# Optimization experiments

Measured on AMD Instinct MI355X. Metric: run time of the kernel, lower is better.

Reference implementation:

```python
import jax, jax.numpy as jnp
import numpy as np

D = 256

def setup_inputs() -> dict:
    key = jax.random.key(0)
    k1, k2, k3, k4, k5, k6 = jax.random.split(key, 6)
    M, N = 2048, 512
    s = 1.0 / np.sqrt(D)
    return {
        "q_vec": jax.random.normal(k1, (M, D), dtype=jnp.float32),
        "kv": jax.random.normal(k2, (M, N, D), dtype=jnp.float32),
        "wq": jax.random.uniform(k3, (D, D), jnp.float32, -s, s),
        "wk": jax.random.uniform(k4, (D, D), jnp.float32, -s, s),
        "wv": jax.random.uniform(k5, (D, D), jnp.float32, -s, s),
        "wo": (jax.random.uniform(k6, (D, D), jnp.float32, -s, s)),
    }

def reference(q_vec, kv, wq, wk, wv, wo):
    # q_vec: [M, d], kv: [M, N, d]; weights stored torch-style [out, in] -> apply x @ W.T
    d = q_vec.shape[-1]
    q = q_vec @ wq.T                          # [M, d]
    k = jnp.einsum('mnd,ed->mne', kv, wk)     # [M, N, d]
    v = jnp.einsum('mnd,ed->mne', kv, wv)     # [M, N, d]
    logits = jnp.einsum('md,mnd->mn', q, k) / jnp.sqrt(jnp.float32(d))  # [M, N]
    attn = jax.nn.softmax(logits, axis=-1)    # [M, N] (dropout p=0.0 is identity)
    ctx = jnp.einsum('mn,mnd->md', attn, v)   # [M, d]
    out = ctx @ wo.T                          # [M, d]
    return out, attn
```

## Files before the change

kernel.cpp:

```cpp
#include <hip/hip_runtime.h>
#include <math.h>

#define DD 256
#define MM 2048
#define NN 512

__global__ void prep_weights(const float* __restrict__ wq, const float* __restrict__ wk,
                             const float* __restrict__ wv, const float* __restrict__ wo,
                             float* __restrict__ B1, float* __restrict__ B2T) {
    __shared__ float sA[DD];
    const int j = threadIdx.x;
    const int b = blockIdx.x;
    if (b < DD) {
        const int d = b;
        sA[j] = wq[j * DD + d];
        __syncthreads();
        float acc = 0.f;
        for (int a = 0; a < DD; ++a) acc = fmaf(sA[a], wk[a * DD + j], acc);
        B1[d * DD + j] = acc * 0.0625f;
    } else {
        const int d = b - DD;
        sA[j] = wv[j * DD + d];
        __syncthreads();
        float acc = 0.f;
        for (int e = 0; e < DD; ++e) acc = fmaf(wo[j * DD + e], sA[e], acc);
        B2T[d * DD + j] = acc;
    }
}

__global__ __launch_bounds__(256, 4)
void attn_fused(const float* __restrict__ q_vec, const float* __restrict__ kv,
                const float* __restrict__ B1, const float* __restrict__ B2T,
                float* __restrict__ out, float* __restrict__ attn_out) {
    __shared__ float s_pe[NN];
    __shared__ float s_lw[16];
    __shared__ float s_wc[16][DD];
    __shared__ float s_q[DD];
    __shared__ float s_qt[DD];

    const int m    = blockIdx.x;
    const int tid  = threadIdx.x;
    const int wave = tid >> 6;
    const int lane = tid & 63;
    const int grp  = lane >> 4;
    const int l16  = lane & 15;

    s_q[tid] = q_vec[(size_t)m * DD + tid];
    __syncthreads();
    {
        float a = 0.f;
#pragma unroll 8
        for (int d = 0; d < DD; ++d) a = fmaf(s_q[d], B1[d * DD + tid], a);
        s_qt[tid] = a;
    }
    __syncthreads();

    const float4* qt4 = (const float4*)s_qt;
    const float4 qv0 = qt4[l16];
    const float4 qv1 = qt4[l16 + 16];
    const float4 qv2 = qt4[l16 + 32];
    const float4 qv3 = qt4[l16 + 48];

    const float4* kv4 = (const float4*)(kv + (size_t)m * NN * DD);
    float4 c0 = make_float4(0.f, 0.f, 0.f, 0.f);
    float4 c1 = c0, c2 = c0, c3 = c0;
    float lw = 0.f;
    const int nbase = wave * 4 + grp;

#pragma unroll 2
    for (int it = 0; it < NN / 16; ++it) {
        const int n = it * 16 + nbase;
        const float4* row = kv4 + (size_t)n * (DD / 4);
        const float4 k0 = row[l16];
        const float4 k1 = row[l16 + 16];
        const float4 k2 = row[l16 + 32];
        const float4 k3 = row[l16 + 48];

        float p;
        p = k0.x * qv0.x;
        p = fmaf(k0.y, qv0.y, p); p = fmaf(k0.z, qv0.z, p); p = fmaf(k0.w, qv0.w, p);
        p = fmaf(k1.x, qv1.x, p); p = fmaf(k1.y, qv1.y, p);
        p = fmaf(k1.z, qv1.z, p); p = fmaf(k1.w, qv1.w, p);
        p = fmaf(k2.x, qv2.x, p); p = fmaf(k2.y, qv2.y, p);
        p = fmaf(k2.z, qv2.z, p); p = fmaf(k2.w, qv2.w, p);
        p = fmaf(k3.x, qv3.x, p); p = fmaf(k3.y, qv3.y, p);
        p = fmaf(k3.z, qv3.z, p); p = fmaf(k3.w, qv3.w, p);

        p += __shfl_xor(p, 1);
        p += __shfl_xor(p, 2);
        p += __shfl_xor(p, 4);
        p += __shfl_xor(p, 8);

        const float pe = __expf(p);
        if (l16 == 0) s_pe[n] = pe;
        lw += pe;

        c0.x = fmaf(pe, k0.x, c0.x); c0.y = fmaf(pe, k0.y, c0.y);
        c0.z = fmaf(pe, k0.z, c0.z); c0.w = fmaf(pe, k0.w, c0.w);
        c1.x = fmaf(pe, k1.x, c1.x); c1.y = fmaf(pe, k1.y, c1.y);
        c1.z = fmaf(pe, k1.z, c1.z); c1.w = fmaf(pe, k1.w, c1.w);
        c2.x = fmaf(pe, k2.x, c2.x); c2.y = fmaf(pe, k2.y, c2.y);
        c2.z = fmaf(pe, k2.z, c2.z); c2.w = fmaf(pe, k2.w, c2.w);
        c3.x = fmaf(pe, k3.x, c3.x); c3.y = fmaf(pe, k3.y, c3.y);
        c3.z = fmaf(pe, k3.z, c3.z); c3.w = fmaf(pe, k3.w, c3.w);
    }

    const int pidx = wave * 4 + grp;
    if (l16 == 0) s_lw[pidx] = lw;
    float4* wc4 = (float4*)(&s_wc[pidx][0]);
    wc4[l16]      = c0;
    wc4[l16 + 16] = c1;
    wc4[l16 + 32] = c2;
    wc4[l16 + 48] = c3;
    __syncthreads();

    float L = 0.f;
#pragma unroll
    for (int i = 0; i < 16; ++i) L += s_lw[i];
    const float invL = 1.f / L;

    float cd = 0.f;
#pragma unroll
    for (int i = 0; i < 16; ++i) cd += s_wc[i][tid];
    cd *= invL;
    __syncthreads();
    s_q[tid] = cd;
    __syncthreads();

    attn_out[(size_t)m * NN + tid]       = s_pe[tid] * invL;
    attn_out[(size_t)m * NN + tid + 256] = s_pe[tid + 256] * invL;

    float o = 0.f;
#pragma unroll 8
    for (int d = 0; d < DD; ++d) o = fmaf(s_q[d], B2T[d * DD + tid], o);
    out[(size_t)m * DD + tid] = o;
}

extern "C" void kernel_launch(void* const* d_in, const int* in_sizes, int n_in,
                              void* d_out, int out_size, void* d_ws, size_t ws_size,
                              hipStream_t stream) {
    const float* q_vec = (const float*)d_in[0];
    const float* kv    = (const float*)d_in[1];
    const float* wq    = (const float*)d_in[2];
    const float* wk    = (const float*)d_in[3];
    const float* wv    = (const float*)d_in[4];
    const float* wo    = (const float*)d_in[5];

    float* out  = (float*)d_out;
    float* attn = (float*)d_out + (size_t)MM * DD;

    float* B1  = (float*)d_ws;
    float* B2T = B1 + DD * DD;

    prep_weights<<<2 * DD, DD, 0, stream>>>(wq, wk, wv, wo, B1, B2T);
    attn_fused<<<MM, DD, 0, stream>>>(q_vec, kv, B1, B2T, out, attn);
}
```

Measured before the change: 242.0 us.

## Prefetch kv rows with nontemporal loads and reduce partial contexts with wave shuffles

The kv streaming loop now software-pipelines its loads: the next row's four float4 values are loaded with nontemporal loads while the current row is processed. The partial context accumulators are first reduced across the four 16-lane groups of each wave with xor shuffles. This shrinks the shared-memory reduction from 16 partials to 4. The prefetch raises register pressure and may reduce occupancy, and the kernel is already bound by HBM bandwidth on kv.

```diff
diff --git a/kernel.cpp b/kernel.cpp
--- a/kernel.cpp
+++ b/kernel.cpp
@@ -4,6 +4,12 @@
 #define DD 256
 #define MM 2048
 #define NN 512
+
+typedef float f32x4 __attribute__((ext_vector_type(4)));
+
+__device__ inline f32x4 ld_nt(const f32x4* p) {
+    return __builtin_nontemporal_load(p);
+}
 
 __global__ void prep_weights(const float* __restrict__ wq, const float* __restrict__ wk,
                              const float* __restrict__ wv, const float* __restrict__ wo,
@@ -33,8 +39,8 @@
                 const float* __restrict__ B1, const float* __restrict__ B2T,
                 float* __restrict__ out, float* __restrict__ attn_out) {
     __shared__ float s_pe[NN];
-    __shared__ float s_lw[16];
-    __shared__ float s_wc[16][DD];
+    __shared__ float s_lw[4];
+    __shared__ float s_wc[4][DD];
     __shared__ float s_q[DD];
     __shared__ float s_qt[DD];
 
@@ -55,73 +61,69 @@
     }
     __syncthreads();
 
-    const float4* qt4 = (const float4*)s_qt;
-    const float4 qv0 = qt4[l16];
-    const float4 qv1 = qt4[l16 + 16];
-    const float4 qv2 = qt4[l16 + 32];
-    const float4 qv3 = qt4[l16 + 48];
+    const f32x4* qt4 = (const f32x4*)s_qt;
+    const f32x4 qv0 = qt4[l16];
+    const f32x4 qv1 = qt4[l16 + 16];
+    const f32x4 qv2 = qt4[l16 + 32];
+    const f32x4 qv3 = qt4[l16 + 48];
 
-    const float4* kv4 = (const float4*)(kv + (size_t)m * NN * DD);
-    float4 c0 = make_float4(0.f, 0.f, 0.f, 0.f);
-    float4 c1 = c0, c2 = c0, c3 = c0;
+    const int nbase = wave * 4 + grp;
+    const f32x4* p = (const f32x4*)(kv + (size_t)m * NN * DD) + (size_t)nbase * 64 + l16;
+    const int STRIDE = 16 * 64;
+
+    f32x4 c0 = (f32x4)0.f, c1 = (f32x4)0.f, c2 = (f32x4)0.f, c3 = (f32x4)0.f;
     float lw = 0.f;
-    const int nbase = wave * 4 + grp;
+
+    f32x4 a0 = ld_nt(p), a1 = ld_nt(p + 16), a2 = ld_nt(p + 32), a3 = ld_nt(p + 48);
 
 #pragma unroll 2
     for (int it = 0; it < NN / 16; ++it) {
-        const int n = it * 16 + nbase;
-        const float4* row = kv4 + (size_t)n * (DD / 4);
-        const float4 k0 = row[l16];
-        const float4 k1 = row[l16 + 16];
-        const float4 k2 = row[l16 + 32];
-        const float4 k3 = row[l16 + 48];
+        f32x4 b0, b1, b2, b3;
+        if (it + 1 < NN / 16) {
+            const f32x4* np = p + (size_t)(it + 1) * STRIDE;
+            b0 = ld_nt(np); b1 = ld_nt(np + 16); b2 = ld_nt(np + 32); b3 = ld_nt(np + 48);
+        }
+        f32x4 t = a0 * qv0 + a1 * qv1 + a2 * qv2 + a3 * qv3;
+        float pdot = (t[0] + t[1]) + (t[2] + t[3]);
+        pdot += __shfl_xor(pdot, 1);
+        pdot += __shfl_xor(pdot, 2);
+        pdot += __shfl_xor(pdot, 4);
+        pdot += __shfl_xor(pdot, 8);
 
-        float p;
-        p = k0.x * qv0.x;
-        p = fmaf(k0.y, qv0.y, p); p = fmaf(k0.z, qv0.z, p); p = fmaf(k0.w, qv0.w, p);
-        p = fmaf(k1.x, qv1.x, p); p = fmaf(k1.y, qv1.y, p);
-        p = fmaf(k1.z, qv1.z, p); p = fmaf(k1.w, qv1.w, p);
-        p = fmaf(k2.x, qv2.x, p); p = fmaf(k2.y, qv2.y, p);
-        p = fmaf(k2.z, qv2.z, p); p = fmaf(k2.w, qv2.w, p);
-        p = fmaf(k3.x, qv3.x, p); p = fmaf(k3.y, qv3.y, p);
-        p = fmaf(k3.z, qv3.z, p); p = fmaf(k3.w, qv3.w, p);
-
-        p += __shfl_xor(p, 1);
-        p += __shfl_xor(p, 2);
-        p += __shfl_xor(p, 4);
-        p += __shfl_xor(p, 8);
-
-        const float pe = __expf(p);
-        if (l16 == 0) s_pe[n] = pe;
+        const float pe = __expf(pdot);
+        if (l16 == 0) s_pe[it * 16 + nbase] = pe;
         lw += pe;
 
-        c0.x = fmaf(pe, k0.x, c0.x); c0.y = fmaf(pe, k0.y, c0.y);
-        c0.z = fmaf(pe, k0.z, c0.z); c0.w = fmaf(pe, k0.w, c0.w);
-        c1.x = fmaf(pe, k1.x, c1.x); c1.y = fmaf(pe, k1.y, c1.y);
-        c1.z = fmaf(pe, k1.z, c1.z); c1.w = fmaf(pe, k1.w, c1.w);
-        c2.x = fmaf(pe, k2.x, c2.x); c2.y = fmaf(pe, k2.y, c2.y);
-        c2.z = fmaf(pe, k2.z, c2.z); c2.w = fmaf(pe, k2.w, c2.w);
-        c3.x = fmaf(pe, k3.x, c3.x); c3.y = fmaf(pe, k3.y, c3.y);
-        c3.z = fmaf(pe, k3.z, c3.z); c3.w = fmaf(pe, k3.w, c3.w);
+        c0 += pe * a0;
+        c1 += pe * a1;
+        c2 += pe * a2;
+        c3 += pe * a3;
+
+        a0 = b0; a1 = b1; a2 = b2; a3 = b3;
     }
 
-    const int pidx = wave * 4 + grp;
-    if (l16 == 0) s_lw[pidx] = lw;
-    float4* wc4 = (float4*)(&s_wc[pidx][0]);
-    wc4[l16]      = c0;
-    wc4[l16 + 16] = c1;
-    wc4[l16 + 32] = c2;
-    wc4[l16 + 48] = c3;
+#pragma unroll
+    for (int i = 0; i < 4; ++i) {
+        c0[i] += __shfl_xor(c0[i], 16); c1[i] += __shfl_xor(c1[i], 16);
+        c2[i] += __shfl_xor(c2[i], 16); c3[i] += __shfl_xor(c3[i], 16);
+        c0[i] += __shfl_xor(c0[i], 32); c1[i] += __shfl_xor(c1[i], 32);
+        c2[i] += __shfl_xor(c2[i], 32); c3[i] += __shfl_xor(c3[i], 32);
+    }
+    lw += __shfl_xor(lw, 16);
+    lw += __shfl_xor(lw, 32);
+
+    {
+        f32x4* wc4 = (f32x4*)(&s_wc[wave][0]);
+        const f32x4 cg = (grp == 0) ? c0 : (grp == 1) ? c1 : (grp == 2) ? c2 : c3;
+        wc4[grp * 16 + l16] = cg;
+        if (lane == 0) s_lw[wave] = lw;
+    }
     __syncthreads();
 
-    float L = 0.f;
-#pragma unroll
-    for (int i = 0; i < 16; ++i) L += s_lw[i];
+    const float L = s_lw[0] + s_lw[1] + s_lw[2] + s_lw[3];
     const float invL = 1.f / L;
 
-    float cd = 0.f;
-#pragma unroll
-    for (int i = 0; i < 16; ++i) cd += s_wc[i][tid];
+    float cd = (s_wc[0][tid] + s_wc[1][tid]) + (s_wc[2][tid] + s_wc[3][tid]);
     cd *= invL;
     __syncthreads();
     s_q[tid] = cd;
```

Result: faster. 208.8 us (-13.7%).
